# Kernel tuning notes

Hardware: AMD Instinct MI355X
Metric: run time of the kernel (lower is better)

Reference implementation:

```python
import jax, jax.numpy as jnp
import numpy as np

N, E, IN, ED, HID, B, K = 50000, 800000, 128, 64, 256, 128, 1000


def setup_inputs() -> dict:
    key = jax.random.key(0)
    ks = jax.random.split(key, 16)

    def lin(k, fi, fo):
        k1, k2 = jax.random.split(k)
        s = 1.0 / np.sqrt(fi)
        return (jax.random.uniform(k1, (fi, fo), jnp.float32, -s, s),
                jax.random.uniform(k2, (fo,), jnp.float32, -s, s))

    We, be = lin(ks[0], ED, IN)        # GINEConv edge projection edge_dim -> in_channels
    W1, b1 = lin(ks[1], IN, HID)       # GINE nn layer 1
    W2, b2 = lin(ks[2], HID, HID)      # GINE nn layer 2
    Wg1, bg1 = lin(ks[3], HID, 128)    # gate_nn layer 1
    Wg2, bg2 = lin(ks[4], 128, 1)      # gate_nn layer 2
    Wh, bh = lin(ks[5], HID, K)        # head

    x = jax.random.normal(ks[6], (N, IN), jnp.float32)
    edge_index = jax.random.randint(ks[7], (2, E), 0, N, jnp.int64)
    edge_attr = jax.random.normal(ks[8], (E, ED), jnp.float32)
    batch = jnp.sort(jax.random.randint(ks[9], (N,), 0, B, jnp.int64))

    return {"x": x, "edge_index": edge_index, "edge_attr": edge_attr, "batch": batch,
            "We": We, "be": be, "W1": W1, "b1": b1, "W2": W2, "b2": b2,
            "Wg1": Wg1, "bg1": bg1, "Wg2": Wg2, "bg2": bg2, "Wh": Wh, "bh": bh}


def reference(x, edge_index, edge_attr, batch, We, be, W1, b1, W2, b2,
              Wg1, bg1, Wg2, bg2, Wh, bh):
    src, dst = edge_index[0], edge_index[1]
    # GINEConv message: ReLU(x_j + Lin(edge_attr)), scatter-add to dst (eps=0)
    e = edge_attr @ We + be                      # [E, IN]
    m = jax.nn.relu(x[src] + e)                  # [E, IN]
    agg = jax.ops.segment_sum(m, dst, num_segments=N)  # [N, IN]
    h = x + agg                                  # (1+eps)*x + agg, eps=0
    h = jax.nn.relu(h @ W1 + b1) @ W2 + b2       # [N, HID]
    # GlobalAttention: segment softmax of gate over graphs, weighted sum
    gate = jax.nn.relu(h @ Wg1 + bg1) @ Wg2 + bg2            # [N, 1]
    gmax = jax.ops.segment_max(gate, batch, num_segments=B)  # [B, 1]
    a = jnp.exp(gate - gmax[batch])
    denom = jax.ops.segment_sum(a, batch, num_segments=B)    # [B, 1]
    attn = a / denom[batch]
    pooled = jax.ops.segment_sum(attn * h, batch, num_segments=B)  # [B, HID]
    logits = pooled @ Wh + bh                    # [B, K]
    return (logits, pooled)
```

## Files before the change

kernel.cpp:

```cpp
#include <hip/hip_runtime.h>
#include <stdint.h>

#define NN    50000
#define EE    800000
#define IN_C  128
#define ED_C  64
#define HID_C 256
#define BB    128
#define KK    1000
#define G1_C  128
#define NV    50176


typedef __attribute__((ext_vector_type(8))) short bfrag;
typedef __attribute__((ext_vector_type(4))) float f4acc;

__device__ __forceinline__ unsigned short f2bs(float f){
  unsigned u = __float_as_uint(f);
  return (unsigned short)((u + 0x7fffu + ((u >> 16) & 1u)) >> 16);
}
__device__ __forceinline__ float bs2f(unsigned short s){
  return __uint_as_float(((unsigned)s) << 16);
}

__device__ __forceinline__ void atomicMaxFloat(float* addr, float val){
  int old = __float_as_int(*addr);
  while (__int_as_float(old) < val){
    int assumed = old;
    old = atomicCAS((int*)addr, assumed, __float_as_int(val));
    if (old == assumed) break;
  }
}

__global__ __launch_bounds__(256) void k_prep(
    const float* __restrict__ We, const float* __restrict__ W1,
    const float* __restrict__ W2, const float* __restrict__ Wg1,
    unsigned short* __restrict__ Wet, unsigned short* __restrict__ W1t,
    unsigned short* __restrict__ W2t, unsigned short* __restrict__ Wg1t)
{
  int i = blockIdx.x * 256 + threadIdx.x;
  if (i < 128 * 64){ int c = i >> 6, k = i & 63;  Wet[i]  = f2bs(We[k * 128 + c]); }
  if (i < 256 * 128){ int n = i >> 7, k = i & 127; W1t[i]  = f2bs(W1[k * 256 + n]); }
  if (i < 256 * 256){ int n = i >> 8, k = i & 255; W2t[i]  = f2bs(W2[k * 256 + n]); }
  if (i < 128 * 256){ int n = i >> 8, k = i & 255; Wg1t[i] = f2bs(Wg1[k * 128 + n]); }
}

__global__ __launch_bounds__(256) void k_xb(const float* __restrict__ x,
                                            unsigned short* __restrict__ xb){
  int i = blockIdx.x * 256 + threadIdx.x;
  if (i < NN * IN_C / 4){
    const float4 v = ((const float4*)x)[i];
    ushort4 o;
    o.x = f2bs(v.x); o.y = f2bs(v.y); o.z = f2bs(v.z); o.w = f2bs(v.w);
    ((ushort4*)xb)[i] = o;
  }
}

__global__ __launch_bounds__(256) void k_init(float* __restrict__ agg,
                                              int* __restrict__ cnt,
                                              int* __restrict__ fill,
                                              int* __restrict__ aux,
                                              float* __restrict__ gmax,
                                              float* __restrict__ denom,
                                              float* __restrict__ pooled){
  size_t i = (size_t)blockIdx.x * 256 + threadIdx.x;
  if (i < (size_t)NN * IN_C) agg[i] = 0.f;
  if (i < NV){ cnt[i] = 0; fill[i] = 0; }
  if (i < 256) aux[i] = 0;
  if (i < BB){ gmax[i] = -1e30f; denom[i] = 0.f; }
  if (i < BB * HID_C) pooled[i] = 0.f;
}

__global__ __launch_bounds__(256) void k_hist(const int* __restrict__ ei,
                                              int* __restrict__ cnt){
  int e = blockIdx.x * 256 + threadIdx.x;
  if (e < EE) atomicAdd(&cnt[ei[EE + e]], 1);
}

__global__ __launch_bounds__(256) void k_scan1(const int* __restrict__ cnt,
                                               int* __restrict__ off,
                                               int* __restrict__ aux){
  __shared__ int s[256];
  int t = threadIdx.x, i = blockIdx.x * 256 + t;
  int val = cnt[i];
  s[t] = val; __syncthreads();
#pragma unroll
  for (int o = 1; o < 256; o <<= 1){
    int v = (t >= o) ? s[t - o] : 0;
    __syncthreads();
    s[t] += v;
    __syncthreads();
  }
  off[i] = s[t] - val;
  if (t == 255) aux[blockIdx.x] = s[255];
}

__global__ __launch_bounds__(256) void k_scan2(int* __restrict__ aux){
  __shared__ int s[256];
  int t = threadIdx.x;
  int val = aux[t];
  s[t] = val; __syncthreads();
#pragma unroll
  for (int o = 1; o < 256; o <<= 1){
    int v = (t >= o) ? s[t - o] : 0;
    __syncthreads();
    s[t] += v;
    __syncthreads();
  }
  aux[t] = s[t] - val;
}

__global__ __launch_bounds__(256) void k_scan3(int* __restrict__ off,
                                               const int* __restrict__ aux){
  int i = blockIdx.x * 256 + threadIdx.x;
  off[i] += aux[blockIdx.x];
}

__global__ __launch_bounds__(256) void k_scatter(const int* __restrict__ ei,
                                                 const int* __restrict__ off,
                                                 int* __restrict__ fill,
                                                 uint4* __restrict__ sorted){
  int e = blockIdx.x * 256 + threadIdx.x;
  if (e < EE){
    int s = ei[e], d = ei[EE + e];
    int pos = off[d] + atomicAdd(&fill[d], 1);
    sorted[pos] = make_uint4((unsigned)e, (unsigned)s, (unsigned)d, 0u);
  }
}

__global__ __launch_bounds__(256, 4) void k_edge2(
    const unsigned short* __restrict__ xb, const uint4* __restrict__ sorted,
    const float* __restrict__ edge_attr,
    const unsigned short* __restrict__ Wet, const float* __restrict__ be,
    float* __restrict__ agg)
{
  __shared__ float msgS[64 * 132];
  __shared__ uint4 sE[64];
  __shared__ int runStart[66];
  __shared__ int nRunsS;
  unsigned short* eaS = (unsigned short*)msgS;

  const int tid = threadIdx.x;
  const int e0 = blockIdx.x * 64;
  if (tid < 64) sE[tid] = sorted[e0 + tid];
  __syncthreads();

  const int lane = tid & 63, wv = tid >> 6;
  const int q = lane >> 4, l15 = lane & 15;
  const int g0 = wv * 16;

  const int xrow = g0 + (lane >> 2);
  const int xc0 = (lane & 3) * 32;
  const unsigned short* xptr = xb + (size_t)((int)sE[xrow].y) * IN_C + xc0;
  uint4 xr[4];
#pragma unroll
  for (int j = 0; j < 4; ++j) xr[j] = *(const uint4*)(xptr + j * 8);

#pragma unroll
  for (int t = 0; t < 4; ++t){
    int f4 = t * 256 + tid;
    int er = f4 >> 4;
    int kk = (f4 & 15) * 4;
    int eid = (int)sE[er].x;
    const float4 v = *(const float4*)(edge_attr + (size_t)eid * ED_C + kk);
    unsigned p0 = (unsigned)f2bs(v.x) | ((unsigned)f2bs(v.y) << 16);
    unsigned p1 = (unsigned)f2bs(v.z) | ((unsigned)f2bs(v.w) << 16);
    *(uint2*)&eaS[er * 72 + kk] = make_uint2(p0, p1);
  }

  if (tid < 64){
    bool flag = (tid == 0) || ((int)sE[tid].z != (int)sE[tid - 1].z);
    unsigned long long m = __ballot(flag);
    int pre = __popcll(m & ((1ull << tid) - 1ull));
    if ((m >> tid) & 1ull) runStart[pre] = tid;
    if (tid == 0){
      int nr = __popcll(m);
      nRunsS = nr;
      runStart[nr] = 64;
    }
  }
  __syncthreads();

  f4acc acc[8];
  const f4acc zz = {0.f, 0.f, 0.f, 0.f};
#pragma unroll
  for (int nt = 0; nt < 8; ++nt) acc[nt] = zz;

#pragma unroll
  for (int ks = 0; ks < 2; ++ks){
    bfrag a = *(const bfrag*)&eaS[(g0 + l15) * 72 + ks * 32 + q * 8];
#pragma unroll
    for (int nt = 0; nt < 8; ++nt){
      int c = nt * 16 + l15;
      bfrag b = *(const bfrag*)(Wet + c * ED_C + ks * 32 + q * 8);
      acc[nt] = __builtin_amdgcn_mfma_f32_16x16x32_bf16(a, b, acc[nt], 0, 0, 0);
    }
  }

  float bev[8];
#pragma unroll
  for (int nt = 0; nt < 8; ++nt) bev[nt] = be[nt * 16 + l15];

  __syncthreads();

#pragma unroll
  for (int nt = 0; nt < 8; ++nt){
    int c = nt * 16 + l15;
#pragma unroll
    for (int r = 0; r < 4; ++r)
      msgS[(g0 + q * 4 + r) * 132 + c] = acc[nt][r] + bev[nt];
  }

  {
    float* mr = &msgS[xrow * 132 + xc0];
#pragma unroll
    for (int jj = 0; jj < 4; ++jj){
      const uint4 u = xr[jj];
      float4 w0 = *(float4*)(mr + jj * 8);
      float4 w1 = *(float4*)(mr + jj * 8 + 4);
      w0.x = fmaxf(w0.x + __uint_as_float(u.x << 16), 0.f);
      w0.y = fmaxf(w0.y + __uint_as_float(u.x & 0xffff0000u), 0.f);
      w0.z = fmaxf(w0.z + __uint_as_float(u.y << 16), 0.f);
      w0.w = fmaxf(w0.w + __uint_as_float(u.y & 0xffff0000u), 0.f);
      w1.x = fmaxf(w1.x + __uint_as_float(u.z << 16), 0.f);
      w1.y = fmaxf(w1.y + __uint_as_float(u.z & 0xffff0000u), 0.f);
      w1.z = fmaxf(w1.z + __uint_as_float(u.w << 16), 0.f);
      w1.w = fmaxf(w1.w + __uint_as_float(u.w & 0xffff0000u), 0.f);
      *(float4*)(mr + jj * 8) = w0;
      *(float4*)(mr + jj * 8 + 4) = w1;
    }
  }
  __syncthreads();

  {
    const int col = tid & 127;
    const int h = tid >> 7;
    const int nR = nRunsS;
    for (int i = h; i < nR; i += 2){
      int s = runStart[i], e = runStart[i + 1];
      int dst = (int)sE[s].z;
      float run = 0.f;
      for (int r = s; r < e; ++r) run += msgS[r * 132 + col];
      size_t a = (size_t)dst * IN_C + col;
      if (s == 0 || e == 64) atomicAdd(&agg[a], run);
      else                   agg[a] = run;
    }
  }
}

__global__ __launch_bounds__(256) void k_h0(const float* __restrict__ agg,
                                            const float* __restrict__ x,
                                            unsigned short* __restrict__ h0b){
  int i = blockIdx.x * 256 + threadIdx.x;
  if (i < NN * IN_C) h0b[i] = f2bs(agg[i] + x[i]);
}

template<int K, bool RELU, bool OF32, bool OB16>
__global__ __launch_bounds__(256) void k_gemm(
    const unsigned short* __restrict__ A, const unsigned short* __restrict__ Wt,
    const float* __restrict__ bias, float* __restrict__ outf,
    unsigned short* __restrict__ outb, int M, int Ntot)
{
  __shared__ unsigned short aS[64 * 40];
  __shared__ unsigned short bS[128 * 40];
  const int tid = threadIdx.x;
  const int lane = tid & 63, wv = tid >> 6;
  const int wi = wv >> 1, wj = wv & 1;
  const int q = lane >> 4, l15 = lane & 15;
  const int mb0 = blockIdx.x * 64;
  const int nb0 = blockIdx.y * 128;
  const int arow = tid >> 2, achk = tid & 3;

  f4acc acc[2][4];
  const f4acc zz = {0.f, 0.f, 0.f, 0.f};
#pragma unroll
  for (int mt = 0; mt < 2; ++mt)
#pragma unroll
    for (int nt = 0; nt < 4; ++nt) acc[mt][nt] = zz;

  for (int ks = 0; ks < K / 32; ++ks){
    {
      int m = mb0 + arow; if (m >= M) m = M - 1;
      const uint4 v = *(const uint4*)(A + (size_t)m * K + ks * 32 + achk * 8);
      *(uint4*)&aS[arow * 40 + achk * 8] = v;
    }
#pragma unroll
    for (int i = 0; i < 2; ++i){
      int idx = i * 256 + tid;
      int row = idx >> 2, chk = idx & 3;
      const uint4 v = *(const uint4*)(Wt + (size_t)(nb0 + row) * K + ks * 32 + chk * 8);
      *(uint4*)&bS[row * 40 + chk * 8] = v;
    }
    __syncthreads();
    bfrag a[2], b[4];
#pragma unroll
    for (int mt = 0; mt < 2; ++mt)
      a[mt] = *(const bfrag*)&aS[(wi * 32 + mt * 16 + l15) * 40 + q * 8];
#pragma unroll
    for (int nt = 0; nt < 4; ++nt)
      b[nt] = *(const bfrag*)&bS[(wj * 64 + nt * 16 + l15) * 40 + q * 8];
#pragma unroll
    for (int mt = 0; mt < 2; ++mt)
#pragma unroll
      for (int nt = 0; nt < 4; ++nt)
        acc[mt][nt] = __builtin_amdgcn_mfma_f32_16x16x32_bf16(a[mt], b[nt], acc[mt][nt], 0, 0, 0);
    __syncthreads();
  }

  const int mb = mb0 + wi * 32;
  const int nb = nb0 + wj * 64;
#pragma unroll
  for (int nt = 0; nt < 4; ++nt){
    int c = nb + nt * 16 + l15;
    float bv = bias[c];
#pragma unroll
    for (int mt = 0; mt < 2; ++mt){
#pragma unroll
      for (int r = 0; r < 4; ++r){
        int m = mb + mt * 16 + q * 4 + r;
        if (m < M){
          float v = acc[mt][nt][r] + bv;
          if (RELU) v = v > 0.f ? v : 0.f;
          if (OF32) outf[(size_t)m * Ntot + c] = v;
          if (OB16) outb[(size_t)m * Ntot + c] = f2bs(v);
        }
      }
    }
  }
}

__global__ __launch_bounds__(256) void k_gate2(const float* __restrict__ g1,
                                               const float* __restrict__ Wg2,
                                               const float* __restrict__ bg2,
                                               float* __restrict__ gate, int nrows){
  const int lane = threadIdx.x & 63, wv = threadIdx.x >> 6;
  const float2 w2 = *(const float2*)(Wg2 + lane * 2);
  const float bg = bg2[0];
  for (int r = blockIdx.x * 4 + wv; r < nrows; r += gridDim.x * 4){
    const float2 a2 = *(const float2*)(g1 + (size_t)r * G1_C + lane * 2);
    float p = a2.x * w2.x + a2.y * w2.y;
#pragma unroll
    for (int off = 32; off > 0; off >>= 1) p += __shfl_down(p, off);
    if (lane == 0) gate[r] = p + bg;
  }
}

__global__ __launch_bounds__(256) void k_gmax(const float* __restrict__ gate,
                                              const int* __restrict__ batch,
                                              float* __restrict__ gmax, int nrows){
  __shared__ float red[256];
  const int tid = threadIdx.x;
  const int n0 = blockIdx.x * 256;
  const int n = n0 + tid;
  const int nlast = (n0 + 255 < nrows) ? n0 + 255 : nrows - 1;
  const int bmin = batch[n0], bmax = batch[nlast];
  float val = -3e38f; int b = bmax;
  if (n < nrows){ b = batch[n]; val = gate[n]; }
  for (int bb = bmin; bb <= bmax; ++bb){
    red[tid] = (b == bb) ? val : -3e38f;
    __syncthreads();
    for (int s = 128; s > 0; s >>= 1){
      if (tid < s) red[tid] = fmaxf(red[tid], red[tid + s]);
      __syncthreads();
    }
    if (tid == 0 && red[0] > -1e37f) atomicMaxFloat(&gmax[bb], red[0]);
    __syncthreads();
  }
}

__global__ __launch_bounds__(256) void k_expsum(const float* __restrict__ gate,
                                                const int* __restrict__ batch,
                                                const float* __restrict__ gmax,
                                                float* __restrict__ aexp,
                                                float* __restrict__ denom, int nrows){
  __shared__ float red[256];
  const int tid = threadIdx.x;
  const int n0 = blockIdx.x * 256;
  const int n = n0 + tid;
  const int nlast = (n0 + 255 < nrows) ? n0 + 255 : nrows - 1;
  const int bmin = batch[n0], bmax = batch[nlast];
  float val = 0.f; int b = bmax;
  if (n < nrows){
    b = batch[n];
    val = expf(gate[n] - gmax[b]);
    aexp[n] = val;
  }
  for (int bb = bmin; bb <= bmax; ++bb){
    red[tid] = (b == bb) ? val : 0.f;
    __syncthreads();
    for (int s = 128; s > 0; s >>= 1){
      if (tid < s) red[tid] += red[tid + s];
      __syncthreads();
    }
    if (tid == 0 && red[0] != 0.f) atomicAdd(&denom[bb], red[0]);
    __syncthreads();
  }
}

__global__ __launch_bounds__(256) void k_pool(const unsigned short* __restrict__ h2b,
                                              const float* __restrict__ aexp,
                                              const float* __restrict__ denom,
                                              const int* __restrict__ batch,
                                              float* __restrict__ pooled, int nrows){
  const int c = threadIdx.x;
  const int n0 = blockIdx.x * 256;
  int n1 = n0 + 256; if (n1 > nrows) n1 = nrows;
  float acc = 0.f;
  int curb = batch[n0];
  for (int n = n0; n < n1; ++n){
    int b = batch[n];
    if (b != curb){
      atomicAdd(&pooled[(size_t)curb * HID_C + c], acc);
      acc = 0.f; curb = b;
    }
    float wgt = aexp[n] / denom[b];
    acc = fmaf(wgt, bs2f(h2b[(size_t)n * HID_C + c]), acc);
  }
  atomicAdd(&pooled[(size_t)curb * HID_C + c], acc);
}

__global__ __launch_bounds__(256) void k_head(const float* __restrict__ pooled,
                                              const float* __restrict__ Wh,
                                              const float* __restrict__ bh,
                                              float* __restrict__ out_logits,
                                              float* __restrict__ out_pooled){
  __shared__ float p[HID_C];
  const int b = blockIdx.x, t = threadIdx.x;
  float pv = pooled[(size_t)b * HID_C + t];
  p[t] = pv;
  out_pooled[(size_t)b * HID_C + t] = pv;
  __syncthreads();
  for (int c = t; c < KK; c += 256){
    float acc = bh[c];
#pragma unroll 8
    for (int k = 0; k < HID_C; ++k)
      acc = fmaf(p[k], Wh[k * KK + c], acc);
    out_logits[(size_t)b * KK + c] = acc;
  }
}

extern "C" void kernel_launch(void* const* d_in, const int* in_sizes, int n_in,
                              void* d_out, int out_size, void* d_ws, size_t ws_size,
                              hipStream_t stream) {
  const float* x   = (const float*)d_in[0];
  const int*   ei  = (const int*)d_in[1];
  const float* ea  = (const float*)d_in[2];
  const int*   batch = (const int*)d_in[3];
  const float* We  = (const float*)d_in[4];
  const float* be  = (const float*)d_in[5];
  const float* W1  = (const float*)d_in[6];
  const float* b1  = (const float*)d_in[7];
  const float* W2  = (const float*)d_in[8];
  const float* b2  = (const float*)d_in[9];
  const float* Wg1 = (const float*)d_in[10];
  const float* bg1 = (const float*)d_in[11];
  const float* Wg2 = (const float*)d_in[12];
  const float* bg2 = (const float*)d_in[13];
  const float* Wh  = (const float*)d_in[14];
  const float* bh  = (const float*)d_in[15];

  float* out_logits = (float*)d_out;
  float* out_pooled = out_logits + (size_t)BB * KK;

  float* agg    = (float*)d_ws;
  float* gate   = agg   + (size_t)NN * IN_C;
  float* aexp   = gate  + NN;
  float* gmax   = aexp  + NN;
  float* denom  = gmax  + BB;
  float* pooled = denom + BB;
  float* fend   = pooled + (size_t)BB * HID_C;
  unsigned short* h0b  = (unsigned short*)fend;
  unsigned short* h1b  = h0b + (size_t)NN * IN_C;
  unsigned short* h2b  = h1b + (size_t)NN * HID_C;
  unsigned short* Wet  = h2b + (size_t)NN * HID_C;
  unsigned short* W1t  = Wet + 128 * 64;
  unsigned short* W2t  = W1t + 256 * 128;
  unsigned short* Wg1t = W2t + 256 * 256;
  unsigned short* xb   = Wg1t + 128 * 256;
  float* g1f = agg;
  uint4* sorted = (uint4*)h1b;
  int* cnt  = (int*)(sorted + EE);
  int* off  = cnt + NV;
  int* fill = off + NV;
  int* aux  = fill + NV;

  k_prep<<<256, 256, 0, stream>>>(We, W1, W2, Wg1, Wet, W1t, W2t, Wg1t);
  k_xb<<<(NN * IN_C / 4 + 255) / 256, 256, 0, stream>>>(x, xb);
  k_init<<<(NN * IN_C + 255) / 256, 256, 0, stream>>>(agg, cnt, fill, aux, gmax, denom, pooled);
  k_hist   <<<(EE + 255) / 256, 256, 0, stream>>>(ei, cnt);
  k_scan1  <<<NV / 256, 256, 0, stream>>>(cnt, off, aux);
  k_scan2  <<<1, 256, 0, stream>>>(aux);
  k_scan3  <<<NV / 256, 256, 0, stream>>>(off, aux);
  k_scatter<<<(EE + 255) / 256, 256, 0, stream>>>(ei, off, fill, sorted);
  k_edge2<<<EE / 64, 256, 0, stream>>>(xb, sorted, ea, Wet, be, agg);
  k_h0<<<(NN * IN_C + 255) / 256, 256, 0, stream>>>(agg, x, h0b);
  k_gemm<128, true,  false, true ><<<dim3(782, 2), 256, 0, stream>>>(h0b, W1t, b1, (float*)0, h1b, NN, HID_C);
  k_gemm<256, false, false, true ><<<dim3(782, 2), 256, 0, stream>>>(h1b, W2t, b2, (float*)0, h2b, NN, HID_C);
  k_gemm<256, true,  true,  false><<<dim3(782, 1), 256, 0, stream>>>(h2b, Wg1t, bg1, g1f, (unsigned short*)0, NN, G1_C);
  k_gate2<<<3125, 256, 0, stream>>>(g1f, Wg2, bg2, gate, NN);
  k_gmax  <<<(NN + 255) / 256, 256, 0, stream>>>(gate, batch, gmax, NN);
  k_expsum<<<(NN + 255) / 256, 256, 0, stream>>>(gate, batch, gmax, aexp, denom, NN);
  k_pool  <<<(NN + 255) / 256, 256, 0, stream>>>(h2b, aexp, denom, batch, pooled, NN);
  k_head<<<BB, 256, 0, stream>>>(pooled, Wh, bh, out_logits, out_pooled);
}
```

Baseline: 739.8 us.

## Fuse setup kernels, fold gate projection into GEMM epilogue, shuffle reductions, finer pooling

Three setup kernels (weight transpose, x to bf16, zero-init) become one launch. The gate second layer (dot with Wg2) moves into the third GEMM's epilogue, so the fp32 g1 intermediate is never written and k_gate2 is gone. The shared-memory tree reductions in gmax and expsum become wave shuffles. k_pool now uses 32-row blocks, giving more parallelism at the cost of more atomics.

After: 666.9 us. 9.9% less time.

```diff
diff --git a/kernel.cpp b/kernel.cpp
--- a/kernel.cpp
+++ b/kernel.cpp
@@ -32,38 +32,28 @@
   }
 }
 
-__global__ __launch_bounds__(256) void k_prep(
+__global__ __launch_bounds__(256) void k_setup(
     const float* __restrict__ We, const float* __restrict__ W1,
     const float* __restrict__ W2, const float* __restrict__ Wg1,
+    const float* __restrict__ x,
     unsigned short* __restrict__ Wet, unsigned short* __restrict__ W1t,
-    unsigned short* __restrict__ W2t, unsigned short* __restrict__ Wg1t)
+    unsigned short* __restrict__ W2t, unsigned short* __restrict__ Wg1t,
+    unsigned short* __restrict__ xb,
+    float* __restrict__ agg, int* __restrict__ cnt, int* __restrict__ fill,
+    int* __restrict__ aux, float* __restrict__ gmax, float* __restrict__ denom,
+    float* __restrict__ pooled)
 {
-  int i = blockIdx.x * 256 + threadIdx.x;
-  if (i < 128 * 64){ int c = i >> 6, k = i & 63;  Wet[i]  = f2bs(We[k * 128 + c]); }
-  if (i < 256 * 128){ int n = i >> 7, k = i & 127; W1t[i]  = f2bs(W1[k * 256 + n]); }
-  if (i < 256 * 256){ int n = i >> 8, k = i & 255; W2t[i]  = f2bs(W2[k * 256 + n]); }
-  if (i < 128 * 256){ int n = i >> 8, k = i & 255; Wg1t[i] = f2bs(Wg1[k * 128 + n]); }
-}
-
-__global__ __launch_bounds__(256) void k_xb(const float* __restrict__ x,
-                                            unsigned short* __restrict__ xb){
-  int i = blockIdx.x * 256 + threadIdx.x;
-  if (i < NN * IN_C / 4){
+  size_t i = (size_t)blockIdx.x * 256 + threadIdx.x;
+  if (i < 128 * 64){ int c = (int)i >> 6, k = (int)i & 63;  Wet[i]  = f2bs(We[k * 128 + c]); }
+  if (i < 256 * 128){ int n = (int)i >> 7, k = (int)i & 127; W1t[i]  = f2bs(W1[k * 256 + n]); }
+  if (i < 256 * 256){ int n = (int)i >> 8, k = (int)i & 255; W2t[i]  = f2bs(W2[k * 256 + n]); }
+  if (i < 128 * 256){ int n = (int)i >> 8, k = (int)i & 255; Wg1t[i] = f2bs(Wg1[k * 128 + n]); }
+  if (i < (size_t)NN * IN_C / 4){
     const float4 v = ((const float4*)x)[i];
     ushort4 o;
     o.x = f2bs(v.x); o.y = f2bs(v.y); o.z = f2bs(v.z); o.w = f2bs(v.w);
     ((ushort4*)xb)[i] = o;
   }
-}
-
-__global__ __launch_bounds__(256) void k_init(float* __restrict__ agg,
-                                              int* __restrict__ cnt,
-                                              int* __restrict__ fill,
-                                              int* __restrict__ aux,
-                                              float* __restrict__ gmax,
-                                              float* __restrict__ denom,
-                                              float* __restrict__ pooled){
-  size_t i = (size_t)blockIdx.x * 256 + threadIdx.x;
   if (i < (size_t)NN * IN_C) agg[i] = 0.f;
   if (i < NV){ cnt[i] = 0; fill[i] = 0; }
   if (i < 256) aux[i] = 0;
@@ -255,14 +245,17 @@
   if (i < NN * IN_C) h0b[i] = f2bs(agg[i] + x[i]);
 }
 
-template<int K, bool RELU, bool OF32, bool OB16>
+template<int K, bool RELU, bool OB16, bool GATE>
 __global__ __launch_bounds__(256) void k_gemm(
     const unsigned short* __restrict__ A, const unsigned short* __restrict__ Wt,
-    const float* __restrict__ bias, float* __restrict__ outf,
-    unsigned short* __restrict__ outb, int M, int Ntot)
+    const float* __restrict__ bias, unsigned short* __restrict__ outb,
+    int M, int Ntot,
+    const float* __restrict__ Wg2, const float* __restrict__ bg2,
+    float* __restrict__ gateOut)
 {
   __shared__ unsigned short aS[64 * 40];
   __shared__ unsigned short bS[128 * 40];
+  __shared__ float gred[2][64];
   const int tid = threadIdx.x;
   const int lane = tid & 63, wv = tid >> 6;
   const int wi = wv >> 1, wj = wv & 1;
@@ -309,61 +302,90 @@
 
   const int mb = mb0 + wi * 32;
   const int nb = nb0 + wj * 64;
-#pragma unroll
-  for (int nt = 0; nt < 4; ++nt){
-    int c = nb + nt * 16 + l15;
-    float bv = bias[c];
-#pragma unroll
-    for (int mt = 0; mt < 2; ++mt){
-#pragma unroll
-      for (int r = 0; r < 4; ++r){
-        int m = mb + mt * 16 + q * 4 + r;
-        if (m < M){
+
+  if (GATE){
+    float wg2v[4];
+#pragma unroll
+    for (int nt = 0; nt < 4; ++nt) wg2v[nt] = Wg2[wj * 64 + nt * 16 + l15];
+    float pr[2][4];
+#pragma unroll
+    for (int mt = 0; mt < 2; ++mt)
+#pragma unroll
+      for (int r = 0; r < 4; ++r) pr[mt][r] = 0.f;
+#pragma unroll
+    for (int nt = 0; nt < 4; ++nt){
+      float bv = bias[wj * 64 + nt * 16 + l15];
+#pragma unroll
+      for (int mt = 0; mt < 2; ++mt)
+#pragma unroll
+        for (int r = 0; r < 4; ++r){
           float v = acc[mt][nt][r] + bv;
-          if (RELU) v = v > 0.f ? v : 0.f;
-          if (OF32) outf[(size_t)m * Ntot + c] = v;
-          if (OB16) outb[(size_t)m * Ntot + c] = f2bs(v);
+          v = v > 0.f ? v : 0.f;
+          pr[mt][r] = fmaf(v, wg2v[nt], pr[mt][r]);
+        }
+    }
+#pragma unroll
+    for (int off = 1; off < 16; off <<= 1)
+#pragma unroll
+      for (int mt = 0; mt < 2; ++mt)
+#pragma unroll
+        for (int r = 0; r < 4; ++r)
+          pr[mt][r] += __shfl_xor(pr[mt][r], off);
+    if (l15 == 0){
+#pragma unroll
+      for (int mt = 0; mt < 2; ++mt)
+#pragma unroll
+        for (int r = 0; r < 4; ++r)
+          gred[wj][wi * 32 + mt * 16 + q * 4 + r] = pr[mt][r];
+    }
+    __syncthreads();
+    if (tid < 64){
+      int m = mb0 + tid;
+      if (m < M) gateOut[m] = gred[0][tid] + gred[1][tid] + bg2[0];
+    }
+  } else {
+#pragma unroll
+    for (int nt = 0; nt < 4; ++nt){
+      int c = nb + nt * 16 + l15;
+      float bv = bias[c];
+#pragma unroll
+      for (int mt = 0; mt < 2; ++mt){
+#pragma unroll
+        for (int r = 0; r < 4; ++r){
+          int m = mb + mt * 16 + q * 4 + r;
+          if (m < M){
+            float v = acc[mt][nt][r] + bv;
+            if (RELU) v = v > 0.f ? v : 0.f;
+            if (OB16) outb[(size_t)m * Ntot + c] = f2bs(v);
+          }
         }
       }
     }
-  }
-}
-
-__global__ __launch_bounds__(256) void k_gate2(const float* __restrict__ g1,
-                                               const float* __restrict__ Wg2,
-                                               const float* __restrict__ bg2,
-                                               float* __restrict__ gate, int nrows){
-  const int lane = threadIdx.x & 63, wv = threadIdx.x >> 6;
-  const float2 w2 = *(const float2*)(Wg2 + lane * 2);
-  const float bg = bg2[0];
-  for (int r = blockIdx.x * 4 + wv; r < nrows; r += gridDim.x * 4){
-    const float2 a2 = *(const float2*)(g1 + (size_t)r * G1_C + lane * 2);
-    float p = a2.x * w2.x + a2.y * w2.y;
-#pragma unroll
-    for (int off = 32; off > 0; off >>= 1) p += __shfl_down(p, off);
-    if (lane == 0) gate[r] = p + bg;
   }
 }
 
 __global__ __launch_bounds__(256) void k_gmax(const float* __restrict__ gate,
                                               const int* __restrict__ batch,
                                               float* __restrict__ gmax, int nrows){
-  __shared__ float red[256];
+  __shared__ float wred[4];
   const int tid = threadIdx.x;
   const int n0 = blockIdx.x * 256;
   const int n = n0 + tid;
   const int nlast = (n0 + 255 < nrows) ? n0 + 255 : nrows - 1;
   const int bmin = batch[n0], bmax = batch[nlast];
+  const int lane = tid & 63, wv = tid >> 6;
   float val = -3e38f; int b = bmax;
   if (n < nrows){ b = batch[n]; val = gate[n]; }
   for (int bb = bmin; bb <= bmax; ++bb){
-    red[tid] = (b == bb) ? val : -3e38f;
-    __syncthreads();
-    for (int s = 128; s > 0; s >>= 1){
-      if (tid < s) red[tid] = fmaxf(red[tid], red[tid + s]);
-      __syncthreads();
-    }
-    if (tid == 0 && red[0] > -1e37f) atomicMaxFloat(&gmax[bb], red[0]);
+    float v = (b == bb) ? val : -3e38f;
+#pragma unroll
+    for (int off = 1; off < 64; off <<= 1) v = fmaxf(v, __shfl_xor(v, off));
+    if (lane == 0) wred[wv] = v;
+    __syncthreads();
+    if (tid == 0){
+      float m = fmaxf(fmaxf(wred[0], wred[1]), fmaxf(wred[2], wred[3]));
+      if (m > -1e37f) atomicMaxFloat(&gmax[bb], m);
+    }
     __syncthreads();
   }
 }
@@ -373,12 +395,13 @@
                                                 const float* __restrict__ gmax,
                                                 float* __restrict__ aexp,
                                                 float* __restrict__ denom, int nrows){
-  __shared__ float red[256];
+  __shared__ float wred[4];
   const int tid = threadIdx.x;
   const int n0 = blockIdx.x * 256;
   const int n = n0 + tid;
   const int nlast = (n0 + 255 < nrows) ? n0 + 255 : nrows - 1;
   const int bmin = batch[n0], bmax = batch[nlast];
+  const int lane = tid & 63, wv = tid >> 6;
   float val = 0.f; int b = bmax;
   if (n < nrows){
     b = batch[n];
@@ -386,13 +409,15 @@
     aexp[n] = val;
   }
   for (int bb = bmin; bb <= bmax; ++bb){
-    red[tid] = (b == bb) ? val : 0.f;
-    __syncthreads();
-    for (int s = 128; s > 0; s >>= 1){
-      if (tid < s) red[tid] += red[tid + s];
-      __syncthreads();
-    }
-    if (tid == 0 && red[0] != 0.f) atomicAdd(&denom[bb], red[0]);
+    float v = (b == bb) ? val : 0.f;
+#pragma unroll
+    for (int off = 1; off < 64; off <<= 1) v += __shfl_xor(v, off);
+    if (lane == 0) wred[wv] = v;
+    __syncthreads();
+    if (tid == 0){
+      float s = wred[0] + wred[1] + wred[2] + wred[3];
+      if (s != 0.f) atomicAdd(&denom[bb], s);
+    }
     __syncthreads();
   }
 }
@@ -403,8 +428,9 @@
                                               const int* __restrict__ batch,
                                               float* __restrict__ pooled, int nrows){
   const int c = threadIdx.x;
-  const int n0 = blockIdx.x * 256;
-  int n1 = n0 + 256; if (n1 > nrows) n1 = nrows;
+  const int n0 = blockIdx.x * 32;
+  int n1 = n0 + 32; if (n1 > nrows) n1 = nrows;
+  if (n0 >= nrows) return;
   float acc = 0.f;
   int curb = batch[n0];
   for (int n = n0; n < n1; ++n){
@@ -477,16 +503,15 @@
   unsigned short* W2t  = W1t + 256 * 128;
   unsigned short* Wg1t = W2t + 256 * 256;
   unsigned short* xb   = Wg1t + 128 * 256;
-  float* g1f = agg;
   uint4* sorted = (uint4*)h1b;
   int* cnt  = (int*)(sorted + EE);
   int* off  = cnt + NV;
   int* fill = off + NV;
   int* aux  = fill + NV;
 
-  k_prep<<<256, 256, 0, stream>>>(We, W1, W2, Wg1, Wet, W1t, W2t, Wg1t);
-  k_xb<<<(NN * IN_C / 4 + 255) / 256, 256, 0, stream>>>(x, xb);
-  k_init<<<(NN * IN_C + 255) / 256, 256, 0, stream>>>(agg, cnt, fill, aux, gmax, denom, pooled);
+  k_setup<<<(NN * IN_C + 255) / 256, 256, 0, stream>>>(
+      We, W1, W2, Wg1, x, Wet, W1t, W2t, Wg1t, xb,
+      agg, cnt, fill, aux, gmax, denom, pooled);
   k_hist   <<<(EE + 255) / 256, 256, 0, stream>>>(ei, cnt);
   k_scan1  <<<NV / 256, 256, 0, stream>>>(cnt, off, aux);
   k_scan2  <<<1, 256, 0, stream>>>(aux);
@@ -494,12 +519,14 @@
   k_scatter<<<(EE + 255) / 256, 256, 0, stream>>>(ei, off, fill, sorted);
   k_edge2<<<EE / 64, 256, 0, stream>>>(xb, sorted, ea, Wet, be, agg);
   k_h0<<<(NN * IN_C + 255) / 256, 256, 0, stream>>>(agg, x, h0b);
-  k_gemm<128, true,  false, true ><<<dim3(782, 2), 256, 0, stream>>>(h0b, W1t, b1, (float*)0, h1b, NN, HID_C);
-  k_gemm<256, false, false, true ><<<dim3(782, 2), 256, 0, stream>>>(h1b, W2t, b2, (float*)0, h2b, NN, HID_C);
-  k_gemm<256, true,  true,  false><<<dim3(782, 1), 256, 0, stream>>>(h2b, Wg1t, bg1, g1f, (unsigned short*)0, NN, G1_C);
-  k_gate2<<<3125, 256, 0, stream>>>(g1f, Wg2, bg2, gate, NN);
+  k_gemm<128, true,  true,  false><<<dim3(782, 2), 256, 0, stream>>>(
+      h0b, W1t, b1, h1b, NN, HID_C, (const float*)0, (const float*)0, (float*)0);
+  k_gemm<256, false, true,  false><<<dim3(782, 2), 256, 0, stream>>>(
+      h1b, W2t, b2, h2b, NN, HID_C, (const float*)0, (const float*)0, (float*)0);
+  k_gemm<256, true,  false, true ><<<dim3(782, 1), 256, 0, stream>>>(
+      h2b, Wg1t, bg1, (unsigned short*)0, NN, G1_C, Wg2, bg2, gate);
   k_gmax  <<<(NN + 255) / 256, 256, 0, stream>>>(gate, batch, gmax, NN);
   k_expsum<<<(NN + 255) / 256, 256, 0, stream>>>(gate, batch, gmax, aexp, denom, NN);
-  k_pool  <<<(NN + 255) / 256, 256, 0, stream>>>(h2b, aexp, denom, batch, pooled, NN);
+  k_pool  <<<(NN + 31) / 32, 256, 0, stream>>>(h2b, aexp, denom, batch, pooled, NN);
   k_head<<<BB, 256, 0, stream>>>(pooled, Wh, bh, out_logits, out_pooled);
 }
```
